# Performance work log

Hardware: AMD Instinct MI355X
Metric: run time of the kernel (lower is better)

The kernel has to match this reference:

```python
import jax, jax.numpy as jnp
import numpy as np

SEQ_LEN = 2048
VOCAB = 32000
EMB = 512
HID = 1024


def setup_inputs() -> dict:
    key = jax.random.key(0)
    ks = jax.random.split(key, 8)
    s = lambda n: 1.0 / np.sqrt(n)
    return {
        "tokens": jax.random.randint(ks[0], (SEQ_LEN,), 0, VOCAB, dtype=jnp.int64 if jax.config.jax_enable_x64 else jnp.int32),
        "embedding_mat": jax.random.normal(ks[1], (VOCAB, EMB), dtype=jnp.float32),
        "W1": jax.random.normal(ks[2], (EMB, HID), dtype=jnp.float32) * s(EMB),
        "U1": jax.random.normal(ks[3], (HID, HID), dtype=jnp.float32) * s(HID),
        "b1": jnp.zeros((HID,), dtype=jnp.float32),
        "W2": jax.random.normal(ks[4], (HID, EMB), dtype=jnp.float32) * s(HID),
        "U2": jax.random.normal(ks[5], (EMB, EMB), dtype=jnp.float32) * s(EMB),
        "b2": jnp.zeros((EMB,), dtype=jnp.float32),
    }


def _rnn_scan(inputs, W1, U1, b1, W2, U2, b2):
    # 2-layer vanilla tanh RNN over time; inputs: [T, EMB] -> outputs: [T, EMB]
    h1_0 = jnp.zeros((W1.shape[1],), dtype=inputs.dtype)
    h2_0 = jnp.zeros((W2.shape[1],), dtype=inputs.dtype)

    def step(carry, x_t):
        h1, h2 = carry
        h1 = jnp.tanh(x_t @ W1 + h1 @ U1 + b1)
        h2 = jnp.tanh(h1 @ W2 + h2 @ U2 + b2)
        return (h1, h2), h2

    _, outs = jax.lax.scan(step, (h1_0, h2_0), inputs)
    return outs


def reference(tokens, embedding_mat, W1, U1, b1, W2, U2, b2):
    # embed tokens, shift right by one (teacher forcing with zero BOS)
    embedded = jnp.take(embedding_mat, tokens, axis=0)          # [T, EMB]
    inputs = jnp.pad(embedded, ((1, 0), (0, 0)))[:-1]           # [T, EMB]
    rnn_outputs = _rnn_scan(inputs, W1, U1, b1, W2, U2, b2)     # [T, EMB]
    logits = rnn_outputs @ embedding_mat.T                      # [T, V]
    raw_log_probs = jax.nn.log_softmax(logits, axis=1)          # [T, V]
    log_probs = jnp.take_along_axis(raw_log_probs, tokens[:, None], axis=1)[:, 0]
    return jnp.sum(log_probs)
```

## Files before the change

kernel.cpp:

```cpp
#include <hip/hip_runtime.h>
#include <stdint.h>


#define TSEQ 2048
#define NVOCAB 32000
#define DEMB 512
#define DHID 1024
#define CAN 0xFFFFFFFFu

typedef __attribute__((ext_vector_type(8))) short short8;
typedef __attribute__((ext_vector_type(4))) float f32x4;
typedef __attribute__((ext_vector_type(2))) float f32x2;
typedef unsigned long long u64;

__device__ __forceinline__ unsigned short f2bf(float f) {
  union { float f; unsigned u; } v; v.f = f;
  unsigned r = (v.u + 0x7FFFu + ((v.u >> 16) & 1u)) >> 16;
  return (unsigned short)r;
}

__device__ __forceinline__ f32x4 llc_ld16(const float* p) {
  f32x4 r;
  asm volatile("global_load_dwordx4 %0, %1, off sc0 sc1\n\ts_waitcnt vmcnt(0)"
               : "=&v"(r) : "v"(p) : "memory");
  return r;
}

__device__ __forceinline__ void llc_ld16_8(const float* pa, const float* pb,
                                           f32x4& a, f32x2& b) {
  asm volatile("global_load_dwordx4 %0, %2, off sc0 sc1\n\t"
               "global_load_dwordx2 %1, %3, off sc0 sc1\n\t"
               "s_waitcnt vmcnt(0)"
               : "=&v"(a), "=&v"(b) : "v"(pa), "v"(pb) : "memory");
}

__device__ __forceinline__ void llc_st4(float* p, float v) {
  asm volatile("global_store_dword %0, %1, off sc0 sc1" :: "v"(p), "v"(v) : "memory");
}

__device__ __forceinline__ bool okq4(f32x4 v) {
  return (__float_as_uint(v.x) != CAN) & (__float_as_uint(v.y) != CAN) &
         (__float_as_uint(v.z) != CAN) & (__float_as_uint(v.w) != CAN);
}
__device__ __forceinline__ bool okp2(f32x2 v) {
  return (__float_as_uint(v.x) != CAN) & (__float_as_uint(v.y) != CAN);
}

__device__ __forceinline__ f32x4 rotq(f32x4 h) {
  f32x4 r;
  r.x = __int_as_float(__builtin_amdgcn_mov_dpp(__float_as_int(h.x), 0x121, 0xf, 0xf, false));
  r.y = __int_as_float(__builtin_amdgcn_mov_dpp(__float_as_int(h.y), 0x121, 0xf, 0xf, false));
  r.z = __int_as_float(__builtin_amdgcn_mov_dpp(__float_as_int(h.z), 0x121, 0xf, 0xf, false));
  r.w = __int_as_float(__builtin_amdgcn_mov_dpp(__float_as_int(h.w), 0x121, 0xf, 0xf, false));
  return r;
}
__device__ __forceinline__ f32x2 rotp(f32x2 h) {
  f32x2 r;
  r.x = __int_as_float(__builtin_amdgcn_mov_dpp(__float_as_int(h.x), 0x121, 0xf, 0xf, false));
  r.y = __int_as_float(__builtin_amdgcn_mov_dpp(__float_as_int(h.y), 0x121, 0xf, 0xf, false));
  return r;
}

__device__ __forceinline__ float tanh_fast(float x) {
  float ax = fabsf(x);
  float e = __expf(ax + ax);
  float t = 1.f - __fdividef(2.f, e + 1.f);
  return (x < 0.f) ? -t : t;
}

__global__ void k_init(uint4* __restrict__ h1v4, uint4* __restrict__ h2v4) {
  const int n1 = (TSEQ + 1) * DHID / 4;
  const int n2 = (TSEQ + 1) * DEMB / 4;
  uint4 can; can.x = CAN; can.y = CAN; can.z = CAN; can.w = CAN;
  uint4 zer; zer.x = 0u; zer.y = 0u; zer.z = 0u; zer.w = 0u;
  const int stride = gridDim.x * blockDim.x;
  for (int i = blockIdx.x * blockDim.x + threadIdx.x; i < n1 + n2; i += stride) {
    if (i < n1) {
      h1v4[i] = (i < DHID / 4) ? zer : can;
    } else {
      int j = i - n1;
      h2v4[j] = (j < DEMB / 4) ? zer : can;
    }
  }
}

__global__ __launch_bounds__(256) void k_xw1(const int* __restrict__ tok,
                                             const float* __restrict__ emb,
                                             const float* __restrict__ W1,
                                             const float* __restrict__ b1,
                                             float* __restrict__ xW1) {
  __shared__ float in_lds[16 * DEMB];
  const int tid = threadIdx.x;
  const int rb = blockIdx.x >> 2, cb = blockIdx.x & 3;
  const int t0 = rb * 16, j0 = cb * 256;
  for (int idx = tid; idx < 16 * 128; idx += 256) {
    int r = idx >> 7, q = idx & 127;
    int t = t0 + r;
    float4 v;
    if (t == 0) { v.x = 0.f; v.y = 0.f; v.z = 0.f; v.w = 0.f; }
    else        { v = *(const float4*)(emb + (size_t)tok[t - 1] * DEMB + q * 4); }
    *(float4*)&in_lds[r * DEMB + q * 4] = v;
  }
  __syncthreads();
  const int j = j0 + tid;
  float acc[16];
  {
    float bb = b1[j];
#pragma unroll
    for (int r = 0; r < 16; ++r) acc[r] = bb;
  }
  for (int k = 0; k < DEMB; k += 4) {
    const float* wp = W1 + (size_t)k * DHID + j;
    float w0 = wp[0], w1 = wp[DHID], w2 = wp[2 * DHID], w3 = wp[3 * DHID];
#pragma unroll
    for (int r = 0; r < 16; ++r) {
      float4 h = *(const float4*)&in_lds[r * DEMB + k];
      acc[r] += h.x * w0;
      acc[r] += h.y * w1;
      acc[r] += h.z * w2;
      acc[r] += h.w * w3;
    }
  }
#pragma unroll
  for (int r = 0; r < 16; ++r) xW1[(size_t)(t0 + r) * DHID + j] = acc[r];
}

__global__ __launch_bounds__(256, 1) void k_rnn(const float* __restrict__ xW1,
                                                const float* __restrict__ U1,
                                                const float* __restrict__ W2,
                                                const float* __restrict__ U2,
                                                const float* __restrict__ b2,
                                                float* __restrict__ h1v,
                                                float* __restrict__ h2v,
                                                float* __restrict__ h2buf) {
  __shared__ float cmb[2][128];
  const int tid = threadIdx.x;
  const int wg = blockIdx.x;
  const int l = tid & 63, w = tid >> 6;
  const int r = l >> 4, i = l & 15;

  if (wg < 64) {
    const int c0 = wg * 16;
    float wA[64];
#pragma unroll
    for (int j = 0; j < 16; ++j) {
      int sl = (i - j) & 15;
      const float* up = U1 + (size_t)(256 * w + 64 * r + 4 * sl) * DHID + c0 + i;
#pragma unroll
      for (int e = 0; e < 4; ++e) wA[4 * j + e] = up[(size_t)e * DHID];
    }
    const float* pp = h1v + 4 * tid;
    const float* xp = xW1 + c0 + (tid & 15);
    float* stp = h1v + DHID + c0 + tid;
    for (int st = 0; st < TSEQ; ++st) {
      float xv = *xp;
      f32x4 h;
      while (true) { h = llc_ld16(pp); if (okq4(h)) break; }
      f32x4 ac = (f32x4)(0.f);
#pragma unroll
      for (int j = 0; j < 16; ++j) {
        ac.x += h.x * wA[4 * j + 0];
        ac.y += h.y * wA[4 * j + 1];
        ac.z += h.z * wA[4 * j + 2];
        ac.w += h.w * wA[4 * j + 3];
        if (j < 15) h = rotq(h);
      }
      float a = (ac.x + ac.y) + (ac.z + ac.w);
      a += __shfl_xor(a, 16);
      a += __shfl_xor(a, 32);
      const int par = st & 1;
      if (l < 16) cmb[par][i * 8 + w] = a;
      __syncthreads();
      if (tid < 16) {
        f32x4 c4 = *(const f32x4*)&cmb[par][tid * 8];
        float hv = tanh_fast(xv + ((c4.x + c4.y) + (c4.z + c4.w)));
        llc_st4(stp, hv);
      }
      pp += DHID; xp += DHID; stp += DHID;
    }
  } else {
    const int c0 = (wg - 64) * 16;
    float wq[64], wp[32];
#pragma unroll
    for (int j = 0; j < 16; ++j) {
      int sl = (i - j) & 15;
      const float* m = W2 + (size_t)(256 * w + 64 * r + 4 * sl) * DEMB + c0 + i;
#pragma unroll
      for (int e = 0; e < 4; ++e) wq[4 * j + e] = m[(size_t)e * DEMB];
      const float* u = U2 + (size_t)(128 * w + 32 * r + 2 * sl) * DEMB + c0 + i;
      wp[2 * j + 0] = u[0];
      wp[2 * j + 1] = u[DEMB];
    }
    const float bias = b2[c0 + (tid & 15)];
    const float* ppA = h1v + DHID + 256 * w + 64 * r + 4 * i;
    const float* ppB = h2v + 128 * w + 32 * r + 2 * i;
    float* stp = h2v + DEMB + c0 + tid;
    float* hb = h2buf + DEMB + c0 + tid;
    for (int t = 0; t < TSEQ; ++t) {
      f32x4 hq; f32x2 hp;
      while (true) {
        llc_ld16_8(ppA, ppB, hq, hp);
        if (okq4(hq) & okp2(hp)) break;
      }
      f32x4 aq = (f32x4)(0.f);
      f32x2 ap = (f32x2)(0.f);
#pragma unroll
      for (int j = 0; j < 16; ++j) {
        aq.x += hq.x * wq[4 * j + 0];
        aq.y += hq.y * wq[4 * j + 1];
        aq.z += hq.z * wq[4 * j + 2];
        aq.w += hq.w * wq[4 * j + 3];
        ap.x += hp.x * wp[2 * j + 0];
        ap.y += hp.y * wp[2 * j + 1];
        if (j < 15) { hq = rotq(hq); hp = rotp(hp); }
      }
      float a = ((aq.x + aq.y) + (aq.z + aq.w)) + (ap.x + ap.y);
      a += __shfl_xor(a, 16);
      a += __shfl_xor(a, 32);
      const int par = t & 1;
      if (l < 16) cmb[par][i * 8 + w] = a;
      __syncthreads();
      if (tid < 16) {
        f32x4 c4 = *(const f32x4*)&cmb[par][tid * 8];
        float hv = tanh_fast(bias + ((c4.x + c4.y) + (c4.z + c4.w)));
        llc_st4(stp, hv);
        *hb = hv;
      }
      ppA += DHID; ppB += DEMB; stp += DEMB; hb += DEMB;
    }
  }
}

__global__ void k_conv(const float* __restrict__ emb, const float* __restrict__ h2f,
                       unsigned short* __restrict__ embB, unsigned short* __restrict__ h2b) {
  const int n1 = NVOCAB * DEMB / 4;
  const int n2 = TSEQ * DEMB / 4;
  const int stride = gridDim.x * blockDim.x;
  for (int i = blockIdx.x * blockDim.x + threadIdx.x; i < n1 + n2; i += stride) {
    float4 v;
    if (i < n1) v = ((const float4*)emb)[i];
    else        v = ((const float4*)h2f)[i - n1];
    ushort4 o;
    o.x = f2bf(v.x); o.y = f2bf(v.y); o.z = f2bf(v.z); o.w = f2bf(v.w);
    if (i < n1) ((ushort4*)embB)[i] = o;
    else        ((ushort4*)h2b)[i - n1] = o;
  }
}

__global__ __launch_bounds__(256, 1) void k_logits(const unsigned short* __restrict__ Ab,
                                                   const unsigned short* __restrict__ Bb,
                                                   float* __restrict__ pmax,
                                                   float* __restrict__ psum) {
  extern __shared__ char smem_dyn[];
  unsigned short* As = (unsigned short*)smem_dyn;
  float* sstat = (float*)(smem_dyn + 131072);
  const int tid = threadIdx.x;
  const int rb = blockIdx.x >> 4, ch = blockIdx.x & 15;
  const int r0 = rb * 128, v0 = ch * 2000;
  for (int idx = tid; idx < 128 * 64; idx += 256) {
    int row = idx >> 6, kq = idx & 63;
    uint4 v = *(const uint4*)(Ab + (size_t)(r0 + row) * DEMB + kq * 8);
    int byte = (row * 1024 + kq * 16) ^ ((row & 7) << 4);
    *(uint4*)((char*)As + byte) = v;
  }
  __syncthreads();
  const int wv = tid >> 6, lane = tid & 63;
  const int col = lane & 15, kg = lane >> 4;
  f32x4 rmax[8], rsum[8];
#pragma unroll
  for (int t = 0; t < 8; ++t) { rmax[t] = (f32x4)(-3.0e38f); rsum[t] = (f32x4)(0.f); }

  for (int strip = wv; strip < 125; strip += 4) {
    const unsigned short* bp = Bb + (size_t)(v0 + strip * 16 + col) * DEMB + kg * 8;
    f32x4 acc[8];
#pragma unroll
    for (int t = 0; t < 8; ++t) acc[t] = (f32x4)(0.f);
#pragma unroll
    for (int ks = 0; ks < 16; ++ks) {
      short8 bfrag = *(const short8*)(bp + ks * 32);
#pragma unroll
      for (int t = 0; t < 8; ++t) {
        int row = t * 16 + col;
        int byte = (row * 1024 + ks * 64 + kg * 16) ^ ((row & 7) << 4);
        short8 afrag = *(const short8*)((const char*)As + byte);
        acc[t] = __builtin_amdgcn_mfma_f32_16x16x32_bf16(afrag, bfrag, acc[t], 0, 0, 0);
      }
    }
#pragma unroll
    for (int t = 0; t < 8; ++t) {
      f32x4 v = acc[t];
      f32x4 mx = v;
#pragma unroll
      for (int d = 1; d < 16; d <<= 1) {
        mx.x = fmaxf(mx.x, __shfl_xor(mx.x, d));
        mx.y = fmaxf(mx.y, __shfl_xor(mx.y, d));
        mx.z = fmaxf(mx.z, __shfl_xor(mx.z, d));
        mx.w = fmaxf(mx.w, __shfl_xor(mx.w, d));
      }
      f32x4 nm;
      nm.x = fmaxf(rmax[t].x, mx.x);
      nm.y = fmaxf(rmax[t].y, mx.y);
      nm.z = fmaxf(rmax[t].z, mx.z);
      nm.w = fmaxf(rmax[t].w, mx.w);
      f32x4 e;
      e.x = __expf(v.x - nm.x); e.y = __expf(v.y - nm.y);
      e.z = __expf(v.z - nm.z); e.w = __expf(v.w - nm.w);
#pragma unroll
      for (int d = 1; d < 16; d <<= 1) {
        e.x += __shfl_xor(e.x, d);
        e.y += __shfl_xor(e.y, d);
        e.z += __shfl_xor(e.z, d);
        e.w += __shfl_xor(e.w, d);
      }
      rsum[t].x = rsum[t].x * __expf(rmax[t].x - nm.x) + e.x;
      rsum[t].y = rsum[t].y * __expf(rmax[t].y - nm.y) + e.y;
      rsum[t].z = rsum[t].z * __expf(rmax[t].z - nm.z) + e.z;
      rsum[t].w = rsum[t].w * __expf(rmax[t].w - nm.w) + e.w;
      rmax[t] = nm;
    }
  }
  if (col == 0) {
#pragma unroll
    for (int t = 0; t < 8; ++t) {
#pragma unroll
      for (int r = 0; r < 4; ++r) {
        int row = t * 16 + kg * 4 + r;
        sstat[(wv * 128 + row) * 2 + 0] = rmax[t][r];
        sstat[(wv * 128 + row) * 2 + 1] = rsum[t][r];
      }
    }
  }
  __syncthreads();
  if (tid < 128) {
    float m = -3.0e38f, ssum = 0.f;
#pragma unroll
    for (int w2 = 0; w2 < 4; ++w2) {
      float pm = sstat[(w2 * 128 + tid) * 2 + 0];
      float ps = sstat[(w2 * 128 + tid) * 2 + 1];
      float nm2 = fmaxf(m, pm);
      ssum = ssum * __expf(m - nm2) + ps * __expf(pm - nm2);
      m = nm2;
    }
    pmax[(size_t)(r0 + tid) * 16 + ch] = m;
    psum[(size_t)(r0 + tid) * 16 + ch] = ssum;
  }
}

__global__ __launch_bounds__(256) void k_tlogit(const int* __restrict__ tok,
                                                const float* __restrict__ emb,
                                                const float* __restrict__ h2buf,
                                                float* __restrict__ tlog) {
  const int wv = threadIdx.x >> 6, lane = threadIdx.x & 63;
  const int wgid = blockIdx.x * 4 + wv;
  for (int t = wgid; t < TSEQ; t += 128) {
    const float* hp = h2buf + (size_t)(t + 1) * DEMB + lane * 8;
    const float* ep = emb + (size_t)tok[t] * DEMB + lane * 8;
    float4 h0 = *(const float4*)hp, h1v = *(const float4*)(hp + 4);
    float4 e0 = *(const float4*)ep, e1v = *(const float4*)(ep + 4);
    float d = h0.x * e0.x + h0.y * e0.y + h0.z * e0.z + h0.w * e0.w +
              h1v.x * e1v.x + h1v.y * e1v.y + h1v.z * e1v.z + h1v.w * e1v.w;
    for (int m = 1; m < 64; m <<= 1) d += __shfl_xor(d, m);
    if (lane == 0) tlog[t] = d;
  }
}

__global__ void k_final(const float* __restrict__ pmax, const float* __restrict__ psum,
                        const float* __restrict__ tlog, float* __restrict__ out) {
  __shared__ float red[4];
  float local = 0.f;
  for (int t = threadIdx.x; t < TSEQ; t += 256) {
    float m = -3.0e38f, s = 0.f;
#pragma unroll
    for (int c = 0; c < 16; ++c) {
      float pm = pmax[t * 16 + c], ps = psum[t * 16 + c];
      float nm = fmaxf(m, pm);
      s = s * __expf(m - nm) + ps * __expf(pm - nm);
      m = nm;
    }
    local += tlog[t] - (m + __logf(s));
  }
  for (int d = 1; d < 64; d <<= 1) local += __shfl_xor(local, d);
  if ((threadIdx.x & 63) == 0) red[threadIdx.x >> 6] = local;
  __syncthreads();
  if (threadIdx.x == 0) out[0] = red[0] + red[1] + red[2] + red[3];
}

extern "C" void kernel_launch(void* const* d_in, const int* in_sizes, int n_in,
                              void* d_out, int out_size, void* d_ws, size_t ws_size,
                              hipStream_t stream) {
  (void)in_sizes; (void)n_in; (void)out_size; (void)ws_size;
  const int*   tok = (const int*)d_in[0];
  const float* emb = (const float*)d_in[1];
  const float* W1  = (const float*)d_in[2];
  const float* U1  = (const float*)d_in[3];
  const float* b1  = (const float*)d_in[4];
  const float* W2  = (const float*)d_in[5];
  const float* U2  = (const float*)d_in[6];
  const float* b2  = (const float*)d_in[7];
  float* out = (float*)d_out;

  char* ws = (char*)d_ws;
  size_t off = 0;
  auto alloc = [&](size_t bytes) {
    char* p = ws + off;
    off = (off + bytes + 255) & ~(size_t)255;
    return p;
  };
  float* h2buf = (float*)alloc((size_t)(TSEQ + 1) * DEMB * 4);
  unsigned short* h2b = (unsigned short*)alloc((size_t)TSEQ * DEMB * 2);
  float* pmax = (float*)alloc((size_t)TSEQ * 16 * 4);
  float* psum = (float*)alloc((size_t)TSEQ * 16 * 4);
  float* tlog = (float*)alloc((size_t)TSEQ * 4);
  size_t sz_h2v = (size_t)(TSEQ + 1) * DEMB * 4;
  size_t sz_h1v = (size_t)(TSEQ + 1) * DHID * 4;
  size_t sz_xw1 = (size_t)TSEQ * DHID * 4;
  size_t sz_embB = (size_t)NVOCAB * DEMB * 2;
  size_t big_sz = sz_h2v + sz_h1v + sz_xw1;
  if (sz_embB > big_sz) big_sz = sz_embB;
  char* big = alloc(big_sz);
  float* h2v = (float*)big;
  float* h1v = (float*)(big + sz_h2v);
  float* xW1 = (float*)(big + sz_h2v + sz_h1v);
  unsigned short* embB = (unsigned short*)big;

  k_init<<<dim3(512), dim3(256), 0, stream>>>((uint4*)h1v, (uint4*)h2v);
  k_xw1<<<dim3(512), dim3(256), 0, stream>>>(tok, emb, W1, b1, xW1);
  k_rnn<<<dim3(96), dim3(256), 0, stream>>>(xW1, U1, W2, U2, b2, h1v, h2v, h2buf);
  k_conv<<<dim3(2048), dim3(256), 0, stream>>>(emb, h2buf + DEMB, embB, h2b);
  k_logits<<<dim3(256), dim3(256), 135168, stream>>>(h2b, embB, pmax, psum);
  k_tlogit<<<dim3(32), dim3(256), 0, stream>>>(tok, emb, h2buf, tlog);
  k_final<<<dim3(1), dim3(256), 0, stream>>>(pmax, psum, tlog, out);
}
```

Measured before the change: 3.810 ms.

## Restructure RNN recurrence into single-wavefront blocks with shuffle-only reductions

The persistent recurrent kernel goes from 96 workgroups of four wavefronts to 256 single-wavefront workgroups. Layer 1 uses 128 blocks with 8 output columns each, and layer 2 uses 128 blocks with 4 columns each. Each lane now loads a contiguous 16-element hidden-state slice with four vector loads, replacing one load plus DPP rotations. Cross-lane reduction is a butterfly of shuffles, removing the per-step LDS write and __syncthreads. This aims to shorten the per-timestep critical path, at the cost of more blocks polling the shared state in L2 and more polling traffic per step.

```diff
diff --git a/kernel.cpp b/kernel.cpp
--- a/kernel.cpp
+++ b/kernel.cpp
@@ -10,7 +10,6 @@
 
 typedef __attribute__((ext_vector_type(8))) short short8;
 typedef __attribute__((ext_vector_type(4))) float f32x4;
-typedef __attribute__((ext_vector_type(2))) float f32x2;
 typedef unsigned long long u64;
 
 __device__ __forceinline__ unsigned short f2bf(float f) {
@@ -19,19 +18,31 @@
   return (unsigned short)r;
 }
 
-__device__ __forceinline__ f32x4 llc_ld16(const float* p) {
-  f32x4 r;
-  asm volatile("global_load_dwordx4 %0, %1, off sc0 sc1\n\ts_waitcnt vmcnt(0)"
-               : "=&v"(r) : "v"(p) : "memory");
-  return r;
-}
-
-__device__ __forceinline__ void llc_ld16_8(const float* pa, const float* pb,
-                                           f32x4& a, f32x2& b) {
-  asm volatile("global_load_dwordx4 %0, %2, off sc0 sc1\n\t"
-               "global_load_dwordx2 %1, %3, off sc0 sc1\n\t"
-               "s_waitcnt vmcnt(0)"
-               : "=&v"(a), "=&v"(b) : "v"(pa), "v"(pb) : "memory");
+__device__ __forceinline__ void llc_ld16x4o(const float* p, f32x4& r0, f32x4& r1,
+                                            f32x4& r2, f32x4& r3) {
+  asm volatile(
+      "global_load_dwordx4 %0, %4, off sc0 sc1\n\t"
+      "global_load_dwordx4 %1, %4, off offset:16 sc0 sc1\n\t"
+      "global_load_dwordx4 %2, %4, off offset:32 sc0 sc1\n\t"
+      "global_load_dwordx4 %3, %4, off offset:48 sc0 sc1\n\t"
+      "s_waitcnt vmcnt(0)"
+      : "=&v"(r0), "=&v"(r1), "=&v"(r2), "=&v"(r3)
+      : "v"(p) : "memory");
+}
+
+__device__ __forceinline__ void llc_ld_l2(const float* pa, const float* pb,
+                                          f32x4& a0, f32x4& a1, f32x4& a2,
+                                          f32x4& a3, f32x4& b0, f32x4& b1) {
+  asm volatile(
+      "global_load_dwordx4 %0, %6, off sc0 sc1\n\t"
+      "global_load_dwordx4 %1, %6, off offset:16 sc0 sc1\n\t"
+      "global_load_dwordx4 %2, %6, off offset:32 sc0 sc1\n\t"
+      "global_load_dwordx4 %3, %6, off offset:48 sc0 sc1\n\t"
+      "global_load_dwordx4 %4, %7, off sc0 sc1\n\t"
+      "global_load_dwordx4 %5, %7, off offset:16 sc0 sc1\n\t"
+      "s_waitcnt vmcnt(0)"
+      : "=&v"(a0), "=&v"(a1), "=&v"(a2), "=&v"(a3), "=&v"(b0), "=&v"(b1)
+      : "v"(pa), "v"(pb) : "memory");
 }
 
 __device__ __forceinline__ void llc_st4(float* p, float v) {
@@ -41,24 +52,6 @@
 __device__ __forceinline__ bool okq4(f32x4 v) {
   return (__float_as_uint(v.x) != CAN) & (__float_as_uint(v.y) != CAN) &
          (__float_as_uint(v.z) != CAN) & (__float_as_uint(v.w) != CAN);
-}
-__device__ __forceinline__ bool okp2(f32x2 v) {
-  return (__float_as_uint(v.x) != CAN) & (__float_as_uint(v.y) != CAN);
-}
-
-__device__ __forceinline__ f32x4 rotq(f32x4 h) {
-  f32x4 r;
-  r.x = __int_as_float(__builtin_amdgcn_mov_dpp(__float_as_int(h.x), 0x121, 0xf, 0xf, false));
-  r.y = __int_as_float(__builtin_amdgcn_mov_dpp(__float_as_int(h.y), 0x121, 0xf, 0xf, false));
-  r.z = __int_as_float(__builtin_amdgcn_mov_dpp(__float_as_int(h.z), 0x121, 0xf, 0xf, false));
-  r.w = __int_as_float(__builtin_amdgcn_mov_dpp(__float_as_int(h.w), 0x121, 0xf, 0xf, false));
-  return r;
-}
-__device__ __forceinline__ f32x2 rotp(f32x2 h) {
-  f32x2 r;
-  r.x = __int_as_float(__builtin_amdgcn_mov_dpp(__float_as_int(h.x), 0x121, 0xf, 0xf, false));
-  r.y = __int_as_float(__builtin_amdgcn_mov_dpp(__float_as_int(h.y), 0x121, 0xf, 0xf, false));
-  return r;
 }
 
 __device__ __forceinline__ float tanh_fast(float x) {
@@ -125,104 +118,130 @@
   for (int r = 0; r < 16; ++r) xW1[(size_t)(t0 + r) * DHID + j] = acc[r];
 }
 
-__global__ __launch_bounds__(256, 1) void k_rnn(const float* __restrict__ xW1,
-                                                const float* __restrict__ U1,
-                                                const float* __restrict__ W2,
-                                                const float* __restrict__ U2,
-                                                const float* __restrict__ b2,
-                                                float* __restrict__ h1v,
-                                                float* __restrict__ h2v,
-                                                float* __restrict__ h2buf) {
-  __shared__ float cmb[2][128];
-  const int tid = threadIdx.x;
+__global__ __launch_bounds__(64, 1) void k_rnn(const float* __restrict__ xW1,
+                                               const float* __restrict__ U1,
+                                               const float* __restrict__ W2,
+                                               const float* __restrict__ U2,
+                                               const float* __restrict__ b2,
+                                               float* __restrict__ h1v,
+                                               float* __restrict__ h2v,
+                                               float* __restrict__ h2buf) {
   const int wg = blockIdx.x;
-  const int l = tid & 63, w = tid >> 6;
-  const int r = l >> 4, i = l & 15;
-
-  if (wg < 64) {
-    const int c0 = wg * 16;
-    float wA[64];
-#pragma unroll
-    for (int j = 0; j < 16; ++j) {
-      int sl = (i - j) & 15;
-      const float* up = U1 + (size_t)(256 * w + 64 * r + 4 * sl) * DHID + c0 + i;
-#pragma unroll
-      for (int e = 0; e < 4; ++e) wA[4 * j + e] = up[(size_t)e * DHID];
-    }
-    const float* pp = h1v + 4 * tid;
-    const float* xp = xW1 + c0 + (tid & 15);
-    float* stp = h1v + DHID + c0 + tid;
+  const int l = threadIdx.x;
+
+  if (wg < 128) {
+    const int c0 = wg * 8;
+    float wA[8][16];
+#pragma unroll
+    for (int kk = 0; kk < 16; ++kk) {
+      const float* up = U1 + (size_t)(16 * l + kk) * DHID + c0;
+#pragma unroll
+      for (int c = 0; c < 8; ++c) wA[c][kk] = up[c];
+    }
+    const int myc = (l >> 3) & 7;
+    const bool hi5 = (l & 32) != 0, hi4 = (l & 16) != 0, hi3 = (l & 8) != 0;
+    const float* pp = h1v + 16 * l;
+    const float* xp = xW1 + c0 + myc;
+    float* stp = h1v + DHID + c0 + myc;
     for (int st = 0; st < TSEQ; ++st) {
       float xv = *xp;
-      f32x4 h;
-      while (true) { h = llc_ld16(pp); if (okq4(h)) break; }
-      f32x4 ac = (f32x4)(0.f);
-#pragma unroll
-      for (int j = 0; j < 16; ++j) {
-        ac.x += h.x * wA[4 * j + 0];
-        ac.y += h.y * wA[4 * j + 1];
-        ac.z += h.z * wA[4 * j + 2];
-        ac.w += h.w * wA[4 * j + 3];
-        if (j < 15) h = rotq(h);
-      }
-      float a = (ac.x + ac.y) + (ac.z + ac.w);
-      a += __shfl_xor(a, 16);
-      a += __shfl_xor(a, 32);
-      const int par = st & 1;
-      if (l < 16) cmb[par][i * 8 + w] = a;
-      __syncthreads();
-      if (tid < 16) {
-        f32x4 c4 = *(const f32x4*)&cmb[par][tid * 8];
-        float hv = tanh_fast(xv + ((c4.x + c4.y) + (c4.z + c4.w)));
-        llc_st4(stp, hv);
-      }
+      f32x4 h0, h1, h2, h3;
+      while (true) {
+        llc_ld16x4o(pp, h0, h1, h2, h3);
+        if (okq4(h0) & okq4(h1) & okq4(h2) & okq4(h3)) break;
+      }
+      float p[8];
+#pragma unroll
+      for (int c = 0; c < 8; ++c) {
+        float s0 = h0.x * wA[c][0] + h0.y * wA[c][1] + h0.z * wA[c][2] + h0.w * wA[c][3];
+        float s1 = h1.x * wA[c][4] + h1.y * wA[c][5] + h1.z * wA[c][6] + h1.w * wA[c][7];
+        float s2 = h2.x * wA[c][8] + h2.y * wA[c][9] + h2.z * wA[c][10] + h2.w * wA[c][11];
+        float s3 = h3.x * wA[c][12] + h3.y * wA[c][13] + h3.z * wA[c][14] + h3.w * wA[c][15];
+        p[c] = (s0 + s1) + (s2 + s3);
+      }
+      float t0 = p[0] + __shfl_xor(p[0], 32);
+      float t1 = p[1] + __shfl_xor(p[1], 32);
+      float t2 = p[2] + __shfl_xor(p[2], 32);
+      float t3 = p[3] + __shfl_xor(p[3], 32);
+      float t4 = p[4] + __shfl_xor(p[4], 32);
+      float t5 = p[5] + __shfl_xor(p[5], 32);
+      float t6 = p[6] + __shfl_xor(p[6], 32);
+      float t7 = p[7] + __shfl_xor(p[7], 32);
+      float a0 = hi5 ? t4 : t0;
+      float a1 = hi5 ? t5 : t1;
+      float a2 = hi5 ? t6 : t2;
+      float a3 = hi5 ? t7 : t3;
+      float u0 = a0 + __shfl_xor(a0, 16);
+      float u1 = a1 + __shfl_xor(a1, 16);
+      float u2 = a2 + __shfl_xor(a2, 16);
+      float u3 = a3 + __shfl_xor(a3, 16);
+      float b0 = hi4 ? u2 : u0;
+      float b1 = hi4 ? u3 : u1;
+      float v0 = b0 + __shfl_xor(b0, 8);
+      float v1 = b1 + __shfl_xor(b1, 8);
+      float cc = hi3 ? v1 : v0;
+      cc += __shfl_xor(cc, 4);
+      cc += __shfl_xor(cc, 2);
+      cc += __shfl_xor(cc, 1);
+      float hv = tanh_fast(xv + cc);
+      if ((l & 7) == 0) llc_st4(stp, hv);
       pp += DHID; xp += DHID; stp += DHID;
     }
   } else {
-    const int c0 = (wg - 64) * 16;
-    float wq[64], wp[32];
-#pragma unroll
-    for (int j = 0; j < 16; ++j) {
-      int sl = (i - j) & 15;
-      const float* m = W2 + (size_t)(256 * w + 64 * r + 4 * sl) * DEMB + c0 + i;
-#pragma unroll
-      for (int e = 0; e < 4; ++e) wq[4 * j + e] = m[(size_t)e * DEMB];
-      const float* u = U2 + (size_t)(128 * w + 32 * r + 2 * sl) * DEMB + c0 + i;
-      wp[2 * j + 0] = u[0];
-      wp[2 * j + 1] = u[DEMB];
-    }
-    const float bias = b2[c0 + (tid & 15)];
-    const float* ppA = h1v + DHID + 256 * w + 64 * r + 4 * i;
-    const float* ppB = h2v + 128 * w + 32 * r + 2 * i;
-    float* stp = h2v + DEMB + c0 + tid;
-    float* hb = h2buf + DEMB + c0 + tid;
+    const int c0 = (wg - 128) * 4;
+    float wq[4][16], wu[4][8];
+#pragma unroll
+    for (int kk = 0; kk < 16; ++kk) {
+      const float* mp = W2 + (size_t)(16 * l + kk) * DEMB + c0;
+#pragma unroll
+      for (int c = 0; c < 4; ++c) wq[c][kk] = mp[c];
+    }
+#pragma unroll
+    for (int kk = 0; kk < 8; ++kk) {
+      const float* up = U2 + (size_t)(8 * l + kk) * DEMB + c0;
+#pragma unroll
+      for (int c = 0; c < 4; ++c) wu[c][kk] = up[c];
+    }
+    const int myc = (l >> 4) & 3;
+    const bool hi5 = (l & 32) != 0, hi4 = (l & 16) != 0;
+    const float bias = b2[c0 + myc];
+    const float* ppA = h1v + DHID + 16 * l;
+    const float* ppB = h2v + 8 * l;
+    float* stp = h2v + DEMB + c0 + myc;
+    float* hb = h2buf + DEMB + c0 + myc;
     for (int t = 0; t < TSEQ; ++t) {
-      f32x4 hq; f32x2 hp;
+      f32x4 a0q, a1q, a2q, a3q, b0q, b1q;
       while (true) {
-        llc_ld16_8(ppA, ppB, hq, hp);
-        if (okq4(hq) & okp2(hp)) break;
-      }
-      f32x4 aq = (f32x4)(0.f);
-      f32x2 ap = (f32x2)(0.f);
-#pragma unroll
-      for (int j = 0; j < 16; ++j) {
-        aq.x += hq.x * wq[4 * j + 0];
-        aq.y += hq.y * wq[4 * j + 1];
-        aq.z += hq.z * wq[4 * j + 2];
-        aq.w += hq.w * wq[4 * j + 3];
-        ap.x += hp.x * wp[2 * j + 0];
-        ap.y += hp.y * wp[2 * j + 1];
-        if (j < 15) { hq = rotq(hq); hp = rotp(hp); }
-      }
-      float a = ((aq.x + aq.y) + (aq.z + aq.w)) + (ap.x + ap.y);
-      a += __shfl_xor(a, 16);
-      a += __shfl_xor(a, 32);
-      const int par = t & 1;
-      if (l < 16) cmb[par][i * 8 + w] = a;
-      __syncthreads();
-      if (tid < 16) {
-        f32x4 c4 = *(const f32x4*)&cmb[par][tid * 8];
-        float hv = tanh_fast(bias + ((c4.x + c4.y) + (c4.z + c4.w)));
+        llc_ld_l2(ppA, ppB, a0q, a1q, a2q, a3q, b0q, b1q);
+        if (okq4(a0q) & okq4(a1q) & okq4(a2q) & okq4(a3q) &
+            okq4(b0q) & okq4(b1q)) break;
+      }
+      float p[4];
+#pragma unroll
+      for (int c = 0; c < 4; ++c) {
+        float s0 = a0q.x * wq[c][0] + a0q.y * wq[c][1] + a0q.z * wq[c][2] + a0q.w * wq[c][3];
+        float s1 = a1q.x * wq[c][4] + a1q.y * wq[c][5] + a1q.z * wq[c][6] + a1q.w * wq[c][7];
+        float s2 = a2q.x * wq[c][8] + a2q.y * wq[c][9] + a2q.z * wq[c][10] + a2q.w * wq[c][11];
+        float s3 = a3q.x * wq[c][12] + a3q.y * wq[c][13] + a3q.z * wq[c][14] + a3q.w * wq[c][15];
+        float s4 = b0q.x * wu[c][0] + b0q.y * wu[c][1] + b0q.z * wu[c][2] + b0q.w * wu[c][3];
+        float s5 = b1q.x * wu[c][4] + b1q.y * wu[c][5] + b1q.z * wu[c][6] + b1q.w * wu[c][7];
+        p[c] = ((s0 + s1) + (s2 + s3)) + (s4 + s5);
+      }
+      float t0 = p[0] + __shfl_xor(p[0], 32);
+      float t1 = p[1] + __shfl_xor(p[1], 32);
+      float t2 = p[2] + __shfl_xor(p[2], 32);
+      float t3 = p[3] + __shfl_xor(p[3], 32);
+      float a0 = hi5 ? t2 : t0;
+      float a1 = hi5 ? t3 : t1;
+      float u0 = a0 + __shfl_xor(a0, 16);
+      float u1 = a1 + __shfl_xor(a1, 16);
+      float q = hi4 ? u1 : u0;
+      q += __shfl_xor(q, 8);
+      q += __shfl_xor(q, 4);
+      q += __shfl_xor(q, 2);
+      q += __shfl_xor(q, 1);
+      float hv = tanh_fast(q + bias);
+      if ((l & 15) == 0) {
         llc_st4(stp, hv);
         *hb = hv;
       }
@@ -425,7 +444,7 @@
 
   k_init<<<dim3(512), dim3(256), 0, stream>>>((uint4*)h1v, (uint4*)h2v);
   k_xw1<<<dim3(512), dim3(256), 0, stream>>>(tok, emb, W1, b1, xW1);
-  k_rnn<<<dim3(96), dim3(256), 0, stream>>>(xW1, U1, W2, U2, b2, h1v, h2v, h2buf);
+  k_rnn<<<dim3(256), dim3(64), 0, stream>>>(xW1, U1, W2, U2, b2, h1v, h2v, h2buf);
   k_conv<<<dim3(2048), dim3(256), 0, stream>>>(emb, h2buf + DEMB, embB, h2b);
   k_logits<<<dim3(256), dim3(256), 135168, stream>>>(h2b, embB, pmax, psum);
   k_tlogit<<<dim3(32), dim3(256), 0, stream>>>(tok, emb, h2buf, tlog);
```

New measurement: 5.506 ms. 44.5% more time.

## Exchange RNN hidden states as packed bf16 and replace barrier with LDS flags

Applied to the files above, without the earlier changes.

Hidden states passed between workgroups through L2/LLC are now stored as packed bf16 pairs, which halves the bytes each polling load and store moves per step. The per-step __syncthreads is replaced by LDS release/acquire flags: waves 1-3 publish their partial sums and wave 0 spins on the flags, then finishes the reduction, tanh and packed store. This shortens the serial critical path of the recurrence, but the recurrent inputs are rounded to bf16 at every step, which loses accuracy. The sentinel polling now checks packed words.

```diff
diff --git a/kernel.cpp b/kernel.cpp
--- a/kernel.cpp
+++ b/kernel.cpp
@@ -11,7 +11,7 @@
 typedef __attribute__((ext_vector_type(8))) short short8;
 typedef __attribute__((ext_vector_type(4))) float f32x4;
 typedef __attribute__((ext_vector_type(2))) float f32x2;
-typedef unsigned long long u64;
+typedef __attribute__((ext_vector_type(2))) unsigned u32x2;
 
 __device__ __forceinline__ unsigned short f2bf(float f) {
   union { float f; unsigned u; } v; v.f = f;
@@ -19,31 +19,30 @@
   return (unsigned short)r;
 }
 
-__device__ __forceinline__ f32x4 llc_ld16(const float* p) {
-  f32x4 r;
-  asm volatile("global_load_dwordx4 %0, %1, off sc0 sc1\n\ts_waitcnt vmcnt(0)"
+__device__ __forceinline__ u32x2 llc_ld8(const unsigned* p) {
+  u32x2 r;
+  asm volatile("global_load_dwordx2 %0, %1, off sc0 sc1\n\ts_waitcnt vmcnt(0)"
                : "=&v"(r) : "v"(p) : "memory");
   return r;
 }
 
-__device__ __forceinline__ void llc_ld16_8(const float* pa, const float* pb,
-                                           f32x4& a, f32x2& b) {
-  asm volatile("global_load_dwordx4 %0, %2, off sc0 sc1\n\t"
-               "global_load_dwordx2 %1, %3, off sc0 sc1\n\t"
+__device__ __forceinline__ void llc_ld8_4(const unsigned* pa, const unsigned* pb,
+                                          u32x2& a, unsigned& b) {
+  asm volatile("global_load_dwordx2 %0, %2, off sc0 sc1\n\t"
+               "global_load_dword %1, %3, off sc0 sc1\n\t"
                "s_waitcnt vmcnt(0)"
                : "=&v"(a), "=&v"(b) : "v"(pa), "v"(pb) : "memory");
 }
 
-__device__ __forceinline__ void llc_st4(float* p, float v) {
+__device__ __forceinline__ void llc_st4u(unsigned* p, unsigned v) {
   asm volatile("global_store_dword %0, %1, off sc0 sc1" :: "v"(p), "v"(v) : "memory");
 }
 
-__device__ __forceinline__ bool okq4(f32x4 v) {
-  return (__float_as_uint(v.x) != CAN) & (__float_as_uint(v.y) != CAN) &
-         (__float_as_uint(v.z) != CAN) & (__float_as_uint(v.w) != CAN);
-}
-__device__ __forceinline__ bool okp2(f32x2 v) {
-  return (__float_as_uint(v.x) != CAN) & (__float_as_uint(v.y) != CAN);
+__device__ __forceinline__ float bflo(unsigned d) {
+  return __uint_as_float(d << 16);
+}
+__device__ __forceinline__ float bfhi(unsigned d) {
+  return __uint_as_float(d & 0xFFFF0000u);
 }
 
 __device__ __forceinline__ f32x4 rotq(f32x4 h) {
@@ -68,18 +67,18 @@
   return (x < 0.f) ? -t : t;
 }
 
-__global__ void k_init(uint4* __restrict__ h1v4, uint4* __restrict__ h2v4) {
-  const int n1 = (TSEQ + 1) * DHID / 4;
-  const int n2 = (TSEQ + 1) * DEMB / 4;
+__global__ void k_init(uint4* __restrict__ h1q, uint4* __restrict__ h2q) {
+  const int n1 = (TSEQ + 1) * DHID * 2 / 16;
+  const int n2 = (TSEQ + 1) * DEMB * 2 / 16;
   uint4 can; can.x = CAN; can.y = CAN; can.z = CAN; can.w = CAN;
   uint4 zer; zer.x = 0u; zer.y = 0u; zer.z = 0u; zer.w = 0u;
   const int stride = gridDim.x * blockDim.x;
   for (int i = blockIdx.x * blockDim.x + threadIdx.x; i < n1 + n2; i += stride) {
     if (i < n1) {
-      h1v4[i] = (i < DHID / 4) ? zer : can;
+      h1q[i] = (i < DHID * 2 / 16) ? zer : can;
     } else {
       int j = i - n1;
-      h2v4[j] = (j < DEMB / 4) ? zer : can;
+      h2q[j] = (j < DEMB * 2 / 16) ? zer : can;
     }
   }
 }
@@ -130,14 +129,17 @@
                                                 const float* __restrict__ W2,
                                                 const float* __restrict__ U2,
                                                 const float* __restrict__ b2,
-                                                float* __restrict__ h1v,
-                                                float* __restrict__ h2v,
+                                                unsigned* __restrict__ h1v,
+                                                unsigned* __restrict__ h2v,
                                                 float* __restrict__ h2buf) {
   __shared__ float cmb[2][128];
+  __shared__ int flg[2][4];
   const int tid = threadIdx.x;
   const int wg = blockIdx.x;
   const int l = tid & 63, w = tid >> 6;
   const int r = l >> 4, i = l & 15;
+  if (tid < 8) flg[tid >> 2][tid & 3] = 0;
+  __syncthreads();
 
   if (wg < 64) {
     const int c0 = wg * 16;
@@ -149,13 +151,16 @@
 #pragma unroll
       for (int e = 0; e < 4; ++e) wA[4 * j + e] = up[(size_t)e * DHID];
     }
-    const float* pp = h1v + 4 * tid;
+    const unsigned* pp = h1v + 2 * tid;
     const float* xp = xW1 + c0 + (tid & 15);
-    float* stp = h1v + DHID + c0 + tid;
+    unsigned* stp = h1v + (DHID / 2) + ((c0 + l) >> 1);
     for (int st = 0; st < TSEQ; ++st) {
       float xv = *xp;
+      u32x2 d;
+      while (true) { d = llc_ld8(pp); if ((d.x != CAN) & (d.y != CAN)) break; }
       f32x4 h;
-      while (true) { h = llc_ld16(pp); if (okq4(h)) break; }
+      h.x = bflo(d.x); h.y = bfhi(d.x);
+      h.z = bflo(d.y); h.w = bfhi(d.y);
       f32x4 ac = (f32x4)(0.f);
 #pragma unroll
       for (int j = 0; j < 16; ++j) {
@@ -169,14 +174,28 @@
       a += __shfl_xor(a, 16);
       a += __shfl_xor(a, 32);
       const int par = st & 1;
-      if (l < 16) cmb[par][i * 8 + w] = a;
-      __syncthreads();
-      if (tid < 16) {
-        f32x4 c4 = *(const f32x4*)&cmb[par][tid * 8];
-        float hv = tanh_fast(xv + ((c4.x + c4.y) + (c4.z + c4.w)));
-        llc_st4(stp, hv);
-      }
-      pp += DHID; xp += DHID; stp += DHID;
+      if (w > 0) {
+        if (l < 16) cmb[par][l * 8 + w] = a;
+        if (l == 0)
+          __hip_atomic_store(&flg[par][w], st + 1, __ATOMIC_RELEASE,
+                             __HIP_MEMORY_SCOPE_WORKGROUP);
+      } else {
+        while (true) {
+          int f1 = __hip_atomic_load(&flg[par][1], __ATOMIC_ACQUIRE, __HIP_MEMORY_SCOPE_WORKGROUP);
+          int f2 = __hip_atomic_load(&flg[par][2], __ATOMIC_ACQUIRE, __HIP_MEMORY_SCOPE_WORKGROUP);
+          int f3 = __hip_atomic_load(&flg[par][3], __ATOMIC_ACQUIRE, __HIP_MEMORY_SCOPE_WORKGROUP);
+          if ((f1 == st + 1) & (f2 == st + 1) & (f3 == st + 1)) break;
+        }
+        f32x4 c4 = *(const f32x4*)&cmb[par][(l & 15) * 8];
+        float s = a + ((c4.y + c4.z) + c4.w);
+        float hv = tanh_fast(xv + s);
+        float hv2 = __shfl_down(hv, 1);
+        if ((l & 1) == 0 && l < 16) {
+          unsigned pk = (unsigned)f2bf(hv) | ((unsigned)f2bf(hv2) << 16);
+          llc_st4u(stp, pk);
+        }
+      }
+      pp += DHID / 2; xp += DHID; stp += DHID / 2;
     }
   } else {
     const int c0 = (wg - 64) * 16;
@@ -192,16 +211,20 @@
       wp[2 * j + 1] = u[DEMB];
     }
     const float bias = b2[c0 + (tid & 15)];
-    const float* ppA = h1v + DHID + 256 * w + 64 * r + 4 * i;
-    const float* ppB = h2v + 128 * w + 32 * r + 2 * i;
-    float* stp = h2v + DEMB + c0 + tid;
-    float* hb = h2buf + DEMB + c0 + tid;
+    const unsigned* ppA = h1v + (DHID / 2) + 128 * w + 32 * r + 2 * i;
+    const unsigned* ppB = h2v + 64 * w + 16 * r + i;
+    unsigned* stp = h2v + (DEMB / 2) + ((c0 + l) >> 1);
+    float* hb = h2buf + DEMB + c0 + l;
     for (int t = 0; t < TSEQ; ++t) {
-      f32x4 hq; f32x2 hp;
+      u32x2 dA; unsigned dB;
       while (true) {
-        llc_ld16_8(ppA, ppB, hq, hp);
-        if (okq4(hq) & okp2(hp)) break;
-      }
+        llc_ld8_4(ppA, ppB, dA, dB);
+        if ((dA.x != CAN) & (dA.y != CAN) & (dB != CAN)) break;
+      }
+      f32x4 hq; f32x2 hp2;
+      hq.x = bflo(dA.x); hq.y = bfhi(dA.x);
+      hq.z = bflo(dA.y); hq.w = bfhi(dA.y);
+      hp2.x = bflo(dB);  hp2.y = bfhi(dB);
       f32x4 aq = (f32x4)(0.f);
       f32x2 ap = (f32x2)(0.f);
 #pragma unroll
@@ -210,23 +233,37 @@
         aq.y += hq.y * wq[4 * j + 1];
         aq.z += hq.z * wq[4 * j + 2];
         aq.w += hq.w * wq[4 * j + 3];
-        ap.x += hp.x * wp[2 * j + 0];
-        ap.y += hp.y * wp[2 * j + 1];
-        if (j < 15) { hq = rotq(hq); hp = rotp(hp); }
+        ap.x += hp2.x * wp[2 * j + 0];
+        ap.y += hp2.y * wp[2 * j + 1];
+        if (j < 15) { hq = rotq(hq); hp2 = rotp(hp2); }
       }
       float a = ((aq.x + aq.y) + (aq.z + aq.w)) + (ap.x + ap.y);
       a += __shfl_xor(a, 16);
       a += __shfl_xor(a, 32);
       const int par = t & 1;
-      if (l < 16) cmb[par][i * 8 + w] = a;
-      __syncthreads();
-      if (tid < 16) {
-        f32x4 c4 = *(const f32x4*)&cmb[par][tid * 8];
-        float hv = tanh_fast(bias + ((c4.x + c4.y) + (c4.z + c4.w)));
-        llc_st4(stp, hv);
-        *hb = hv;
-      }
-      ppA += DHID; ppB += DEMB; stp += DEMB; hb += DEMB;
+      if (w > 0) {
+        if (l < 16) cmb[par][l * 8 + w] = a;
+        if (l == 0)
+          __hip_atomic_store(&flg[par][w], t + 1, __ATOMIC_RELEASE,
+                             __HIP_MEMORY_SCOPE_WORKGROUP);
+      } else {
+        while (true) {
+          int f1 = __hip_atomic_load(&flg[par][1], __ATOMIC_ACQUIRE, __HIP_MEMORY_SCOPE_WORKGROUP);
+          int f2 = __hip_atomic_load(&flg[par][2], __ATOMIC_ACQUIRE, __HIP_MEMORY_SCOPE_WORKGROUP);
+          int f3 = __hip_atomic_load(&flg[par][3], __ATOMIC_ACQUIRE, __HIP_MEMORY_SCOPE_WORKGROUP);
+          if ((f1 == t + 1) & (f2 == t + 1) & (f3 == t + 1)) break;
+        }
+        f32x4 c4 = *(const f32x4*)&cmb[par][(l & 15) * 8];
+        float s = a + ((c4.y + c4.z) + c4.w);
+        float hv = tanh_fast(s + bias);
+        float hv2 = __shfl_down(hv, 1);
+        if (l < 16) *hb = hv;
+        if ((l & 1) == 0 && l < 16) {
+          unsigned pk = (unsigned)f2bf(hv) | ((unsigned)f2bf(hv2) << 16);
+          llc_st4u(stp, pk);
+        }
+      }
+      ppA += DHID / 2; ppB += DEMB / 2; stp += DEMB / 2; hb += DEMB;
     }
   }
 }
@@ -411,15 +448,15 @@
   float* pmax = (float*)alloc((size_t)TSEQ * 16 * 4);
   float* psum = (float*)alloc((size_t)TSEQ * 16 * 4);
   float* tlog = (float*)alloc((size_t)TSEQ * 4);
-  size_t sz_h2v = (size_t)(TSEQ + 1) * DEMB * 4;
-  size_t sz_h1v = (size_t)(TSEQ + 1) * DHID * 4;
+  size_t sz_h2v = (size_t)(TSEQ + 1) * DEMB * 2;
+  size_t sz_h1v = (size_t)(TSEQ + 1) * DHID * 2;
   size_t sz_xw1 = (size_t)TSEQ * DHID * 4;
   size_t sz_embB = (size_t)NVOCAB * DEMB * 2;
   size_t big_sz = sz_h2v + sz_h1v + sz_xw1;
   if (sz_embB > big_sz) big_sz = sz_embB;
   char* big = alloc(big_sz);
-  float* h2v = (float*)big;
-  float* h1v = (float*)(big + sz_h2v);
+  unsigned* h2v = (unsigned*)big;
+  unsigned* h1v = (unsigned*)(big + sz_h2v);
   float* xW1 = (float*)(big + sz_h2v + sz_h1v);
   unsigned short* embB = (unsigned short*)big;
 
```

After: 4.578 ms. 20.1% more time.
